# Kernel optimization log

Hardware: AMD Instinct MI355X
Metric: run time of the kernel (lower is better)

## Reference

```python
import jax, jax.numpy as jnp
import numpy as np

IM_SIZE = (256, 256)
OVERSAMP = 1.25
WIDTH = 6
BETA = float(np.pi * np.sqrt((WIDTH / OVERSAMP * (OVERSAMP - 0.5)) ** 2 - 0.8))
OS_SIZE = tuple(int(np.ceil(OVERSAMP * n)) for n in IM_SIZE)  # (320, 320)
D = 2


def _kb(x):
    # Kaiser-Bessel interpolation kernel: i0(beta*sqrt(1-x^2)) for |x|<=1 (sigpy convention)
    return jnp.i0(BETA * jnp.sqrt(jnp.maximum(1.0 - x * x, 0.0)))


def setup_inputs() -> dict:
    key = jax.random.key(0)
    k1, k2, k3 = jax.random.split(key, 3)
    N, C = 1, 8
    img_r = jax.random.normal(k1, (N, C) + IM_SIZE, dtype=jnp.float32)
    img_i = jax.random.normal(k2, (N, C) + IM_SIZE, dtype=jnp.float32)
    # trajectory in [-N_i/2, N_i/2] per the class docstring
    trj = (jax.random.uniform(k3, (N, 64, 4096, D), dtype=jnp.float32) - 0.5) * 256.0
    return {"img_r": img_r, "img_i": img_i, "trj": trj}


def _nufft_forward(img_r, img_i, trj):
    img = (img_r + 1j * img_i).astype(jnp.complex64)  # (N, C, H, W)
    nd = img.ndim
    # --- apodization (inverse FT of KB kernel), separable per axis ---
    for a in range(D):
        n, osn = IM_SIZE[a], OS_SIZE[a]
        idx = jnp.arange(n, dtype=jnp.float32)
        arg = jnp.sqrt(BETA ** 2 - (np.pi * WIDTH * (idx - n // 2) / osn) ** 2)
        apod = arg / jnp.sinh(arg)
        shape = [1] * nd
        shape[nd - D + a] = n
        img = img * apod.reshape(shape)
    # --- scale + centered zero-pad to oversampled grid ---
    img = img / np.sqrt(float(np.prod(IM_SIZE)))
    pads = [(0, 0)] * (nd - D) + [(((o - n) // 2), (o - n) - ((o - n) // 2))
                                  for n, o in zip(IM_SIZE, OS_SIZE)]
    img = jnp.pad(img, pads)
    # --- centered FFT (ifftshift -> fftn(norm=None) -> fftshift) ---
    axes = tuple(range(-D, 0))
    ksp_os = jnp.fft.fftshift(jnp.fft.fftn(jnp.fft.ifftshift(img, axes=axes), axes=axes), axes=axes)
    # --- scale trajectory to oversampled grid coordinates ---
    scale = jnp.array([OS_SIZE[a] / IM_SIZE[a] for a in range(D)], jnp.float32)
    shift = jnp.array([OS_SIZE[a] // 2 for a in range(D)], jnp.float32)
    coord = trj * scale + shift  # (N, R, S, 2)
    x0 = jnp.ceil(coord - WIDTH / 2.0)
    # --- KB interpolation: fixed 6x6 neighbor loop, vectorized gather over all points ---
    N = img.shape[0]
    out = jnp.zeros((N,) + img.shape[1:nd - D] + coord.shape[1:-1], jnp.complex64)

    def gather(grid, ix, iy):  # grid (C, Hos, Wos), ix/iy (R, S) -> (C, R, S)
        return grid[:, ix, iy]

    for dx in range(WIDTH):
        px = x0[..., 0] + dx
        wx = _kb((px - coord[..., 0]) / (WIDTH / 2.0))
        ix = px.astype(jnp.int32) % OS_SIZE[0]
        for dy in range(WIDTH):
            py = x0[..., 1] + dy
            wy = _kb((py - coord[..., 1]) / (WIDTH / 2.0))
            iy = py.astype(jnp.int32) % OS_SIZE[1]
            vals = jax.vmap(gather)(ksp_os, ix, iy)  # (N, C, R, S)
            out = out + vals * (wx * wy)[:, None, :, :]
    return out / (WIDTH ** D)


def reference(img_r, img_i, trj):
    return _nufft_forward(img_r, img_i, trj)
```

## Files before the change

kernel.cpp:

```cpp
#include <hip/hip_runtime.h>
#include <math.h>

#define NCH   8
#define IMN   256
#define OSN   320
#define NPTS  (64*4096)
#define KD    512
#define BETA_F   10.9551078f
#define BETA2_F  120.014389f
#define APOD_C   0.05890486225f
#define GROWS 326
#define GCOLS 328
#define GPITCH (GCOLS * NCH)

typedef unsigned short u16;
typedef unsigned int   u32;
typedef __attribute__((ext_vector_type(8))) short s16x8;
typedef __attribute__((ext_vector_type(4))) float f32x4;
typedef __attribute__((ext_vector_type(2))) float f32x2;

__device__ __forceinline__ u32 f2bf(float f) {
    u32 u = __float_as_uint(f);
    return (u + 0x7FFFu + ((u >> 16) & 1u)) >> 16;
}

__device__ __forceinline__ float i0f(float t) {
    if (t < 3.75f) {
        float y = t * t * (1.0f / 14.0625f);
        return 1.0f + y * (3.5156229f + y * (3.0899424f + y * (1.2067492f +
                     y * (0.2659732f + y * (0.0360768f + y * 0.0045813f)))));
    }
    float z = 3.75f / t;
    float p = 0.39894228f + z * (0.01328592f + z * (0.00225319f + z * (-0.00157565f +
              z * (0.00916281f + z * (-0.02057706f + z * (0.02635537f +
              z * (-0.01647633f + z * 0.00392377f)))))));
    return expf(t) * rsqrtf(t) * p;
}

__device__ __forceinline__ float apodf(int i) {
    float x = APOD_C * (float)(i - IMN / 2);
    float arg = sqrtf(BETA2_F - x * x);
    float e = expf(arg);
    float sh = 0.5f * (e - 1.0f / e);
    return arg / sh;
}

__global__ void prep(const float* __restrict__ r, const float* __restrict__ im,
                     u32* __restrict__ B1, u32* __restrict__ B2,
                     u32* __restrict__ A) {
    const int b = blockIdx.x, t = threadIdx.x;
    if (b < (OSN * IMN) / 256) {
        int idx = b * 256 + t;
        int k = idx >> 8, j = idx & 255;
        int p = (k * (j + 32)) % OSN;
        float th = (2.0f * (float)M_PI / (float)OSN) * (float)p;
        float s = ((k + j) & 1) ? -1.0f : 1.0f;
        float sn, cs;
        sincosf(th, &sn, &cs);
        float re = s * cs, imv = -s * sn;
        B1[idx] = f2bf(re) | (f2bf(-imv) << 16);
        B2[idx] = f2bf(imv) | (f2bf(re) << 16);
    } else {
        int idx = (b - (OSN * IMN) / 256) * 256 + t;
        int i2 = idx & 255, i1 = (idx >> 8) & 255;
        float w = apodf(i1) * apodf(i2) * (1.0f / 256.0f);
        A[idx] = f2bf(r[idx] * w) | (f2bf(im[idx] * w) << 16);
    }
}

__launch_bounds__(64)
__global__ void gemm1(const short* __restrict__ Abf, const short* __restrict__ B1,
                      const short* __restrict__ B2, short* __restrict__ Tb) {
    const int c = blockIdx.z;
    const int mBase = blockIdx.y * 32;
    const int nBase = blockIdx.x * 32;
    __shared__ short As[2][32][36], B1s[2][32][36], B2s[2][32][36];
    const int t = threadIdx.x;
    const int row = t >> 1, seg = (t & 1) * 16;
    const int fm = t & 15, fq = (t >> 4) * 8;
    const short* ap  = Abf + (long)(c * IMN + mBase + row) * KD + seg;
    const short* b1p = B1 + (long)(nBase + row) * KD + seg;
    const short* b2p = B2 + (long)(nBase + row) * KD + seg;
    f32x4 zz = {0.f, 0.f, 0.f, 0.f};
    f32x4 accRe[2][2], accIm[2][2];
    #pragma unroll
    for (int i = 0; i < 2; i++)
        #pragma unroll
        for (int j = 0; j < 2; j++) { accRe[i][j] = zz; accIm[i][j] = zz; }

    s16x8 c0 = *(const s16x8*)(ap);
    s16x8 c1 = *(const s16x8*)(ap + 8);
    s16x8 c2 = *(const s16x8*)(b1p);
    s16x8 c3 = *(const s16x8*)(b1p + 8);
    s16x8 c4 = *(const s16x8*)(b2p);
    s16x8 c5 = *(const s16x8*)(b2p + 8);

    #pragma unroll
    for (int kc = 0; kc < 16; kc++) {
        const int buf = kc & 1;
        *(s16x8*)&As [buf][row][seg]     = c0;
        *(s16x8*)&As [buf][row][seg + 8] = c1;
        *(s16x8*)&B1s[buf][row][seg]     = c2;
        *(s16x8*)&B1s[buf][row][seg + 8] = c3;
        *(s16x8*)&B2s[buf][row][seg]     = c4;
        *(s16x8*)&B2s[buf][row][seg + 8] = c5;
        if (kc < 15) {
            const int kb = (kc + 1) * 32;
            c0 = *(const s16x8*)(ap + kb);
            c1 = *(const s16x8*)(ap + kb + 8);
            c2 = *(const s16x8*)(b1p + kb);
            c3 = *(const s16x8*)(b1p + kb + 8);
            c4 = *(const s16x8*)(b2p + kb);
            c5 = *(const s16x8*)(b2p + kb + 8);
        }
        s16x8 a0  = *(const s16x8*)&As [buf][fm][fq];
        s16x8 a1  = *(const s16x8*)&As [buf][16 + fm][fq];
        s16x8 b10 = *(const s16x8*)&B1s[buf][fm][fq];
        s16x8 b11 = *(const s16x8*)&B1s[buf][16 + fm][fq];
        s16x8 b20 = *(const s16x8*)&B2s[buf][fm][fq];
        s16x8 b21 = *(const s16x8*)&B2s[buf][16 + fm][fq];
        accRe[0][0] = __builtin_amdgcn_mfma_f32_16x16x32_bf16(a0, b10, accRe[0][0], 0, 0, 0);
        accRe[0][1] = __builtin_amdgcn_mfma_f32_16x16x32_bf16(a0, b11, accRe[0][1], 0, 0, 0);
        accRe[1][0] = __builtin_amdgcn_mfma_f32_16x16x32_bf16(a1, b10, accRe[1][0], 0, 0, 0);
        accRe[1][1] = __builtin_amdgcn_mfma_f32_16x16x32_bf16(a1, b11, accRe[1][1], 0, 0, 0);
        accIm[0][0] = __builtin_amdgcn_mfma_f32_16x16x32_bf16(a0, b20, accIm[0][0], 0, 0, 0);
        accIm[0][1] = __builtin_amdgcn_mfma_f32_16x16x32_bf16(a0, b21, accIm[0][1], 0, 0, 0);
        accIm[1][0] = __builtin_amdgcn_mfma_f32_16x16x32_bf16(a1, b20, accIm[1][0], 0, 0, 0);
        accIm[1][1] = __builtin_amdgcn_mfma_f32_16x16x32_bf16(a1, b21, accIm[1][1], 0, 0, 0);
    }
    #pragma unroll
    for (int i = 0; i < 2; i++)
        #pragma unroll
        for (int j = 0; j < 2; j++) {
            int i1b = mBase + i * 16 + (t >> 4) * 4;
            int k2  = nBase + j * 16 + fm;
            s16x8 v;
            #pragma unroll
            for (int r = 0; r < 4; r++) {
                v[2 * r]     = (short)f2bf(accRe[i][j][r]);
                v[2 * r + 1] = (short)f2bf(accIm[i][j][r]);
            }
            *(s16x8*)(Tb + ((long)(c * OSN + k2)) * KD + 2 * i1b) = v;
        }
}

__launch_bounds__(64)
__global__ void gemm2(const short* __restrict__ B1, const short* __restrict__ B2,
                      const short* __restrict__ Tb, u32* __restrict__ Gb) {
    const int c = blockIdx.z;
    const int mBase = blockIdx.y * 32;
    const int nBase = blockIdx.x * 32;
    __shared__ short A1s[2][32][36], A2s[2][32][36], Bs[2][32][36];
    const int t = threadIdx.x;
    const int row = t >> 1, seg = (t & 1) * 16;
    const int fm = t & 15, fq = (t >> 4) * 8;
    const short* a1p = B1 + (long)(mBase + row) * KD + seg;
    const short* a2p = B2 + (long)(mBase + row) * KD + seg;
    const short* bp  = Tb + ((long)(c * OSN + nBase + row)) * KD + seg;
    f32x4 zz = {0.f, 0.f, 0.f, 0.f};
    f32x4 accRe[2][2], accIm[2][2];
    #pragma unroll
    for (int i = 0; i < 2; i++)
        #pragma unroll
        for (int j = 0; j < 2; j++) { accRe[i][j] = zz; accIm[i][j] = zz; }

    s16x8 c0 = *(const s16x8*)(a1p);
    s16x8 c1 = *(const s16x8*)(a1p + 8);
    s16x8 c2 = *(const s16x8*)(a2p);
    s16x8 c3 = *(const s16x8*)(a2p + 8);
    s16x8 c4 = *(const s16x8*)(bp);
    s16x8 c5 = *(const s16x8*)(bp + 8);

    #pragma unroll
    for (int kc = 0; kc < 16; kc++) {
        const int buf = kc & 1;
        *(s16x8*)&A1s[buf][row][seg]     = c0;
        *(s16x8*)&A1s[buf][row][seg + 8] = c1;
        *(s16x8*)&A2s[buf][row][seg]     = c2;
        *(s16x8*)&A2s[buf][row][seg + 8] = c3;
        *(s16x8*)&Bs [buf][row][seg]     = c4;
        *(s16x8*)&Bs [buf][row][seg + 8] = c5;
        if (kc < 15) {
            const int kb = (kc + 1) * 32;
            c0 = *(const s16x8*)(a1p + kb);
            c1 = *(const s16x8*)(a1p + kb + 8);
            c2 = *(const s16x8*)(a2p + kb);
            c3 = *(const s16x8*)(a2p + kb + 8);
            c4 = *(const s16x8*)(bp + kb);
            c5 = *(const s16x8*)(bp + kb + 8);
        }
        s16x8 a10 = *(const s16x8*)&A1s[buf][fm][fq];
        s16x8 a11 = *(const s16x8*)&A1s[buf][16 + fm][fq];
        s16x8 a20 = *(const s16x8*)&A2s[buf][fm][fq];
        s16x8 a21 = *(const s16x8*)&A2s[buf][16 + fm][fq];
        s16x8 b0  = *(const s16x8*)&Bs [buf][fm][fq];
        s16x8 b1  = *(const s16x8*)&Bs [buf][16 + fm][fq];
        accRe[0][0] = __builtin_amdgcn_mfma_f32_16x16x32_bf16(a10, b0, accRe[0][0], 0, 0, 0);
        accRe[0][1] = __builtin_amdgcn_mfma_f32_16x16x32_bf16(a10, b1, accRe[0][1], 0, 0, 0);
        accRe[1][0] = __builtin_amdgcn_mfma_f32_16x16x32_bf16(a11, b0, accRe[1][0], 0, 0, 0);
        accRe[1][1] = __builtin_amdgcn_mfma_f32_16x16x32_bf16(a11, b1, accRe[1][1], 0, 0, 0);
        accIm[0][0] = __builtin_amdgcn_mfma_f32_16x16x32_bf16(a20, b0, accIm[0][0], 0, 0, 0);
        accIm[0][1] = __builtin_amdgcn_mfma_f32_16x16x32_bf16(a20, b1, accIm[0][1], 0, 0, 0);
        accIm[1][0] = __builtin_amdgcn_mfma_f32_16x16x32_bf16(a21, b0, accIm[1][0], 0, 0, 0);
        accIm[1][1] = __builtin_amdgcn_mfma_f32_16x16x32_bf16(a21, b1, accIm[1][1], 0, 0, 0);
    }
    #pragma unroll
    for (int i = 0; i < 2; i++)
        #pragma unroll
        for (int j = 0; j < 2; j++) {
            int k2 = nBase + j * 16 + fm;
            int pc  = k2 + 3;
            int pc2 = (k2 < 3) ? (k2 + 323) : ((k2 >= 317) ? (k2 - 317) : -1);
            #pragma unroll
            for (int r = 0; r < 4; r++) {
                int k1 = mBase + i * 16 + (t >> 4) * 4 + r;
                u32 val = f2bf(accRe[i][j][r]) | (f2bf(accIm[i][j][r]) << 16);
                int pr  = k1 + 3;
                int pr2 = (k1 < 3) ? (k1 + 323) : ((k1 >= 317) ? (k1 - 317) : -1);
                Gb[(long)pr * GPITCH + pc * NCH + c] = val;
                if (pr2 >= 0)              Gb[(long)pr2 * GPITCH + pc  * NCH + c] = val;
                if (pc2 >= 0)              Gb[(long)pr  * GPITCH + pc2 * NCH + c] = val;
                if (pr2 >= 0 && pc2 >= 0)  Gb[(long)pr2 * GPITCH + pc2 * NCH + c] = val;
            }
        }
}

__launch_bounds__(256, 4)
__global__ void interp_kernel(const float* __restrict__ trj,
                              const u32* __restrict__ grid,
                              u32* __restrict__ out) {
    const int t = threadIdx.x;
    __shared__ float wxs[64][6], wys[64][6];
    __shared__ int   x0s[64], y0s[64];

    if (t < 128) {
        int ptl = t & 63, axis = t >> 6;
        int pt = blockIdx.x * 64 + ptl;
        float tv = trj[pt * 2 + axis];
        float cc = __fadd_rn(__fmul_rn(tv, 1.25f), 160.0f);
        float v0 = ceilf(__fadd_rn(cc, -3.0f));
        if (axis) y0s[ptl] = (int)v0; else x0s[ptl] = (int)v0;
        float* ws = axis ? wys[ptl] : wxs[ptl];
        #pragma unroll
        for (int d = 0; d < 6; d++) {
            float u = __fdiv_rn(__fsub_rn(v0 + (float)d, cc), 3.0f);
            ws[d] = i0f(BETA_F * sqrtf(fmaxf(1.0f - u * u, 0.0f)));
        }
    }
    __syncthreads();

    const int pl = t >> 2;
    const int cp = (t & 3) * 2;
    const int px = x0s[pl] + 3;
    const int py = y0s[pl] + 3;
    const u32* g0 = grid + (long)px * GPITCH + py * NCH + cp;

    uint2 g[36];
    #pragma unroll
    for (int dx = 0; dx < 6; dx++)
        #pragma unroll
        for (int dy = 0; dy < 6; dy++)
            g[dx * 6 + dy] = *(const uint2*)(g0 + dx * GPITCH + dy * NCH);

    float wx[6], wy[6];
    #pragma unroll
    for (int d = 0; d < 6; d++) { wx[d] = wxs[pl][d]; wy[d] = wys[pl][d]; }

    float re0 = 0.f, im0 = 0.f, re1 = 0.f, im1 = 0.f;
    #pragma unroll
    for (int dx = 0; dx < 6; dx++) {
        float wxv = wx[dx];
        #pragma unroll
        for (int dy = 0; dy < 6; dy++) {
            uint2 gv = g[dx * 6 + dy];
            float ww = wxv * wy[dy];
            re0 += __uint_as_float(gv.x << 16) * ww;
            im0 += __uint_as_float(gv.x & 0xFFFF0000u) * ww;
            re1 += __uint_as_float(gv.y << 16) * ww;
            im1 += __uint_as_float(gv.y & 0xFFFF0000u) * ww;
        }
    }
    re0 *= (1.0f / 36.0f); im0 *= (1.0f / 36.0f);
    re1 *= (1.0f / 36.0f); im1 *= (1.0f / 36.0f);

    __shared__ float2 lds[64][9];
    lds[pl][cp]     = make_float2(re0, im0);
    lds[pl][cp + 1] = make_float2(re1, im1);
    __syncthreads();
    int c2 = t >> 5, p2 = t & 31;
    float2 va = lds[p2][c2];
    float2 vb = lds[p2 + 32][c2];
    long ob = (long)c2 * NPTS + blockIdx.x * 64;
    out[ob + p2]      = f2bf(va.y) | (f2bf(va.x) << 16);
    out[ob + p2 + 32] = f2bf(vb.y) | (f2bf(vb.x) << 16);
}

extern "C" void kernel_launch(void* const* d_in, const int* in_sizes, int n_in,
                              void* d_out, int out_size, void* d_ws, size_t ws_size,
                              hipStream_t stream) {
    const float* img_r = (const float*)d_in[0];
    const float* img_i = (const float*)d_in[1];
    const float* trj   = (const float*)d_in[2];

    char* ob = (char*)d_out;
    short* Tb  = (short*)(ob);
    u32*  B1u  = (u32*)(ob + 2621440);
    u32*  B2u  = (u32*)(ob + 2949120);
    u32*  Au   = (u32*)(ob + 3276800);
    u32*  Gb   = (u32*)d_ws;

    prep<<<(OSN * IMN) / 256 + (NCH * IMN * IMN) / 256, 256, 0, stream>>>(
        img_r, img_i, B1u, B2u, Au);
    gemm1<<<dim3(OSN / 32, IMN / 32, NCH), 64, 0, stream>>>(
        (const short*)Au, (const short*)B1u, (const short*)B2u, Tb);
    gemm2<<<dim3(OSN / 32, OSN / 32, NCH), 64, 0, stream>>>(
        (const short*)B1u, (const short*)B2u, Tb, Gb);
    interp_kernel<<<NPTS / 64, 256, 0, stream>>>(trj, Gb, (u32*)d_out);
}
```

Measured before the change: 111.7 us.

## Load MFMA operands directly from global memory and widen interpolation gathers

Both DFT GEMM kernels drop the LDS double-buffer staging. Each lane now loads its MFMA fragments straight from global memory, which removes LDS stores and loads and the associated scheduling overhead but relies on cache reuse across blocks. The interpolation kernel now has each thread gather 16-byte chunks covering four channels over half of the 6x6 stencil. It uses packed f32x2 FMAs and combines the two halves with a cross-lane shuffle. This halves the gather count per thread at the cost of an extra shuffle reduction.

Measured after the change: 117.3 us. +5.0%, slower.

```diff
diff --git a/kernel.cpp b/kernel.cpp
--- a/kernel.cpp
+++ b/kernel.cpp
@@ -74,13 +74,14 @@
     const int c = blockIdx.z;
     const int mBase = blockIdx.y * 32;
     const int nBase = blockIdx.x * 32;
-    __shared__ short As[2][32][36], B1s[2][32][36], B2s[2][32][36];
     const int t = threadIdx.x;
-    const int row = t >> 1, seg = (t & 1) * 16;
     const int fm = t & 15, fq = (t >> 4) * 8;
-    const short* ap  = Abf + (long)(c * IMN + mBase + row) * KD + seg;
-    const short* b1p = B1 + (long)(nBase + row) * KD + seg;
-    const short* b2p = B2 + (long)(nBase + row) * KD + seg;
+    const short* pa0  = Abf + (long)(c * IMN + mBase + fm) * KD + fq;
+    const short* pa1  = pa0 + 16 * KD;
+    const short* pb10 = B1 + (long)(nBase + fm) * KD + fq;
+    const short* pb11 = pb10 + 16 * KD;
+    const short* pb20 = B2 + (long)(nBase + fm) * KD + fq;
+    const short* pb21 = pb20 + 16 * KD;
     f32x4 zz = {0.f, 0.f, 0.f, 0.f};
     f32x4 accRe[2][2], accIm[2][2];
     #pragma unroll
@@ -88,37 +89,15 @@
         #pragma unroll
         for (int j = 0; j < 2; j++) { accRe[i][j] = zz; accIm[i][j] = zz; }
 
-    s16x8 c0 = *(const s16x8*)(ap);
-    s16x8 c1 = *(const s16x8*)(ap + 8);
-    s16x8 c2 = *(const s16x8*)(b1p);
-    s16x8 c3 = *(const s16x8*)(b1p + 8);
-    s16x8 c4 = *(const s16x8*)(b2p);
-    s16x8 c5 = *(const s16x8*)(b2p + 8);
-
     #pragma unroll
     for (int kc = 0; kc < 16; kc++) {
-        const int buf = kc & 1;
-        *(s16x8*)&As [buf][row][seg]     = c0;
-        *(s16x8*)&As [buf][row][seg + 8] = c1;
-        *(s16x8*)&B1s[buf][row][seg]     = c2;
-        *(s16x8*)&B1s[buf][row][seg + 8] = c3;
-        *(s16x8*)&B2s[buf][row][seg]     = c4;
-        *(s16x8*)&B2s[buf][row][seg + 8] = c5;
-        if (kc < 15) {
-            const int kb = (kc + 1) * 32;
-            c0 = *(const s16x8*)(ap + kb);
-            c1 = *(const s16x8*)(ap + kb + 8);
-            c2 = *(const s16x8*)(b1p + kb);
-            c3 = *(const s16x8*)(b1p + kb + 8);
-            c4 = *(const s16x8*)(b2p + kb);
-            c5 = *(const s16x8*)(b2p + kb + 8);
-        }
-        s16x8 a0  = *(const s16x8*)&As [buf][fm][fq];
-        s16x8 a1  = *(const s16x8*)&As [buf][16 + fm][fq];
-        s16x8 b10 = *(const s16x8*)&B1s[buf][fm][fq];
-        s16x8 b11 = *(const s16x8*)&B1s[buf][16 + fm][fq];
-        s16x8 b20 = *(const s16x8*)&B2s[buf][fm][fq];
-        s16x8 b21 = *(const s16x8*)&B2s[buf][16 + fm][fq];
+        const int kb = kc * 32;
+        s16x8 a0  = *(const s16x8*)(pa0  + kb);
+        s16x8 a1  = *(const s16x8*)(pa1  + kb);
+        s16x8 b10 = *(const s16x8*)(pb10 + kb);
+        s16x8 b11 = *(const s16x8*)(pb11 + kb);
+        s16x8 b20 = *(const s16x8*)(pb20 + kb);
+        s16x8 b21 = *(const s16x8*)(pb21 + kb);
         accRe[0][0] = __builtin_amdgcn_mfma_f32_16x16x32_bf16(a0, b10, accRe[0][0], 0, 0, 0);
         accRe[0][1] = __builtin_amdgcn_mfma_f32_16x16x32_bf16(a0, b11, accRe[0][1], 0, 0, 0);
         accRe[1][0] = __builtin_amdgcn_mfma_f32_16x16x32_bf16(a1, b10, accRe[1][0], 0, 0, 0);
@@ -150,13 +129,14 @@
     const int c = blockIdx.z;
     const int mBase = blockIdx.y * 32;
     const int nBase = blockIdx.x * 32;
-    __shared__ short A1s[2][32][36], A2s[2][32][36], Bs[2][32][36];
     const int t = threadIdx.x;
-    const int row = t >> 1, seg = (t & 1) * 16;
     const int fm = t & 15, fq = (t >> 4) * 8;
-    const short* a1p = B1 + (long)(mBase + row) * KD + seg;
-    const short* a2p = B2 + (long)(mBase + row) * KD + seg;
-    const short* bp  = Tb + ((long)(c * OSN + nBase + row)) * KD + seg;
+    const short* pa10 = B1 + (long)(mBase + fm) * KD + fq;
+    const short* pa11 = pa10 + 16 * KD;
+    const short* pa20 = B2 + (long)(mBase + fm) * KD + fq;
+    const short* pa21 = pa20 + 16 * KD;
+    const short* pb0  = Tb + ((long)(c * OSN + nBase + fm)) * KD + fq;
+    const short* pb1  = pb0 + 16 * KD;
     f32x4 zz = {0.f, 0.f, 0.f, 0.f};
     f32x4 accRe[2][2], accIm[2][2];
     #pragma unroll
@@ -164,37 +144,15 @@
         #pragma unroll
         for (int j = 0; j < 2; j++) { accRe[i][j] = zz; accIm[i][j] = zz; }
 
-    s16x8 c0 = *(const s16x8*)(a1p);
-    s16x8 c1 = *(const s16x8*)(a1p + 8);
-    s16x8 c2 = *(const s16x8*)(a2p);
-    s16x8 c3 = *(const s16x8*)(a2p + 8);
-    s16x8 c4 = *(const s16x8*)(bp);
-    s16x8 c5 = *(const s16x8*)(bp + 8);
-
     #pragma unroll
     for (int kc = 0; kc < 16; kc++) {
-        const int buf = kc & 1;
-        *(s16x8*)&A1s[buf][row][seg]     = c0;
-        *(s16x8*)&A1s[buf][row][seg + 8] = c1;
-        *(s16x8*)&A2s[buf][row][seg]     = c2;
-        *(s16x8*)&A2s[buf][row][seg + 8] = c3;
-        *(s16x8*)&Bs [buf][row][seg]     = c4;
-        *(s16x8*)&Bs [buf][row][seg + 8] = c5;
-        if (kc < 15) {
-            const int kb = (kc + 1) * 32;
-            c0 = *(const s16x8*)(a1p + kb);
-            c1 = *(const s16x8*)(a1p + kb + 8);
-            c2 = *(const s16x8*)(a2p + kb);
-            c3 = *(const s16x8*)(a2p + kb + 8);
-            c4 = *(const s16x8*)(bp + kb);
-            c5 = *(const s16x8*)(bp + kb + 8);
-        }
-        s16x8 a10 = *(const s16x8*)&A1s[buf][fm][fq];
-        s16x8 a11 = *(const s16x8*)&A1s[buf][16 + fm][fq];
-        s16x8 a20 = *(const s16x8*)&A2s[buf][fm][fq];
-        s16x8 a21 = *(const s16x8*)&A2s[buf][16 + fm][fq];
-        s16x8 b0  = *(const s16x8*)&Bs [buf][fm][fq];
-        s16x8 b1  = *(const s16x8*)&Bs [buf][16 + fm][fq];
+        const int kb = kc * 32;
+        s16x8 a10 = *(const s16x8*)(pa10 + kb);
+        s16x8 a11 = *(const s16x8*)(pa11 + kb);
+        s16x8 a20 = *(const s16x8*)(pa20 + kb);
+        s16x8 a21 = *(const s16x8*)(pa21 + kb);
+        s16x8 b0  = *(const s16x8*)(pb0  + kb);
+        s16x8 b1  = *(const s16x8*)(pb1  + kb);
         accRe[0][0] = __builtin_amdgcn_mfma_f32_16x16x32_bf16(a10, b0, accRe[0][0], 0, 0, 0);
         accRe[0][1] = __builtin_amdgcn_mfma_f32_16x16x32_bf16(a10, b1, accRe[0][1], 0, 0, 0);
         accRe[1][0] = __builtin_amdgcn_mfma_f32_16x16x32_bf16(a11, b0, accRe[1][0], 0, 0, 0);
@@ -249,43 +207,59 @@
     }
     __syncthreads();
 
-    const int pl = t >> 2;
-    const int cp = (t & 3) * 2;
-    const int px = x0s[pl] + 3;
+    const int pl   = t >> 2;
+    const int cp4  = (t & 1) * 4;
+    const int half = (t >> 1) & 1;
+    const int px = x0s[pl] + 3 + half * 3;
     const int py = y0s[pl] + 3;
-    const u32* g0 = grid + (long)px * GPITCH + py * NCH + cp;
-
-    uint2 g[36];
-    #pragma unroll
-    for (int dx = 0; dx < 6; dx++)
+    const u32* g0 = grid + (long)px * GPITCH + py * NCH + cp4;
+
+    uint4 g[18];
+    #pragma unroll
+    for (int dx = 0; dx < 3; dx++)
         #pragma unroll
         for (int dy = 0; dy < 6; dy++)
-            g[dx * 6 + dy] = *(const uint2*)(g0 + dx * GPITCH + dy * NCH);
-
-    float wx[6], wy[6];
-    #pragma unroll
-    for (int d = 0; d < 6; d++) { wx[d] = wxs[pl][d]; wy[d] = wys[pl][d]; }
-
-    float re0 = 0.f, im0 = 0.f, re1 = 0.f, im1 = 0.f;
-    #pragma unroll
-    for (int dx = 0; dx < 6; dx++) {
+            g[dx * 6 + dy] = *(const uint4*)(g0 + dx * GPITCH + dy * NCH);
+
+    float wx[3], wy[6];
+    #pragma unroll
+    for (int d = 0; d < 3; d++) wx[d] = wxs[pl][half * 3 + d];
+    #pragma unroll
+    for (int d = 0; d < 6; d++) wy[d] = wys[pl][d];
+
+    f32x2 a0 = {0.f, 0.f}, a1 = {0.f, 0.f}, a2 = {0.f, 0.f}, a3 = {0.f, 0.f};
+    #pragma unroll
+    for (int dx = 0; dx < 3; dx++) {
         float wxv = wx[dx];
         #pragma unroll
         for (int dy = 0; dy < 6; dy++) {
-            uint2 gv = g[dx * 6 + dy];
+            uint4 gv = g[dx * 6 + dy];
             float ww = wxv * wy[dy];
-            re0 += __uint_as_float(gv.x << 16) * ww;
-            im0 += __uint_as_float(gv.x & 0xFFFF0000u) * ww;
-            re1 += __uint_as_float(gv.y << 16) * ww;
-            im1 += __uint_as_float(gv.y & 0xFFFF0000u) * ww;
-        }
-    }
-    re0 *= (1.0f / 36.0f); im0 *= (1.0f / 36.0f);
-    re1 *= (1.0f / 36.0f); im1 *= (1.0f / 36.0f);
+            f32x2 w2 = {ww, ww};
+            f32x2 v0v = { __uint_as_float(gv.x << 16), __uint_as_float(gv.x & 0xFFFF0000u) };
+            f32x2 v1v = { __uint_as_float(gv.y << 16), __uint_as_float(gv.y & 0xFFFF0000u) };
+            f32x2 v2v = { __uint_as_float(gv.z << 16), __uint_as_float(gv.z & 0xFFFF0000u) };
+            f32x2 v3v = { __uint_as_float(gv.w << 16), __uint_as_float(gv.w & 0xFFFF0000u) };
+            a0 += v0v * w2;
+            a1 += v1v * w2;
+            a2 += v2v * w2;
+            a3 += v3v * w2;
+        }
+    }
+    a0.x += __shfl_xor(a0.x, 2, 64); a0.y += __shfl_xor(a0.y, 2, 64);
+    a1.x += __shfl_xor(a1.x, 2, 64); a1.y += __shfl_xor(a1.y, 2, 64);
+    a2.x += __shfl_xor(a2.x, 2, 64); a2.y += __shfl_xor(a2.y, 2, 64);
+    a3.x += __shfl_xor(a3.x, 2, 64); a3.y += __shfl_xor(a3.y, 2, 64);
+    f32x2 sc = {1.0f / 36.0f, 1.0f / 36.0f};
+    a0 *= sc; a1 *= sc; a2 *= sc; a3 *= sc;
 
     __shared__ float2 lds[64][9];
-    lds[pl][cp]     = make_float2(re0, im0);
-    lds[pl][cp + 1] = make_float2(re1, im1);
+    if (half == 0) {
+        lds[pl][cp4]     = make_float2(a0.x, a0.y);
+        lds[pl][cp4 + 1] = make_float2(a1.x, a1.y);
+        lds[pl][cp4 + 2] = make_float2(a2.x, a2.y);
+        lds[pl][cp4 + 3] = make_float2(a3.x, a3.y);
+    }
     __syncthreads();
     int c2 = t >> 5, p2 = t & 31;
     float2 va = lds[p2][c2];
```
